# Optimization experiments

Hardware: AMD Instinct MI355X
Metric: run time of the kernel (lower is better)

Reference implementation:

```python
import jax, jax.numpy as jnp
import numpy as np

S, B, E, H, Q, T, K, N = 256, 32, 768, 1024, 64, 512, 11, 16
STD = 2.5
EPS = 1e-5


def gaussian_kernel(size, std):
    t = np.linspace(-(size - 1) / 2, (size - 1) / 2, size)
    x, y = np.meshgrid(t, t)
    kern = np.exp(-0.5 * (x ** 2 + y ** 2) / std ** 2)
    return (kern / kern.sum()).astype(np.float32)


def setup_inputs() -> dict:
    key = jax.random.key(0)
    ks = jax.random.split(key, 24)
    s = 0.05
    inp = {
        'sentence_batch': jax.random.normal(ks[0], (S, B, E), jnp.float32),
        # forward LSTM params (torch layout: W_ih (4H,E), W_hh (4H,H), gate order i,f,g,o)
        'Wih_f': jax.random.normal(ks[1], (4 * H, E), jnp.float32) * s,
        'Whh_f': jax.random.normal(ks[2], (4 * H, H), jnp.float32) * s,
        'bih_f': jnp.zeros((4 * H,), jnp.float32),
        'bhh_f': jnp.zeros((4 * H,), jnp.float32),
        # backward LSTM params
        'Wih_b': jax.random.normal(ks[3], (4 * H, E), jnp.float32) * s,
        'Whh_b': jax.random.normal(ks[4], (4 * H, H), jnp.float32) * s,
        'bih_b': jnp.zeros((4 * H,), jnp.float32),
        'bhh_b': jnp.zeros((4 * H,), jnp.float32),
        # layer norms
        'g_in': jnp.ones((E,), jnp.float32), 'be_in': jnp.zeros((E,), jnp.float32),
        'g_fw': jnp.ones((H,), jnp.float32), 'be_fw': jnp.zeros((H,), jnp.float32),
        'g_bk': jnp.ones((H,), jnp.float32), 'be_bk': jnp.zeros((H,), jnp.float32),
        'g_sq': jnp.ones((2 * Q,), jnp.float32), 'be_sq': jnp.zeros((2 * Q,), jnp.float32),
        # squeeze + topic linears (torch layout: W (out,in))
        'Wsq': jax.random.normal(ks[5], (Q, H), jnp.float32) * s,
        'bsq': jnp.zeros((Q,), jnp.float32),
        'Wtop': jax.random.normal(ks[6], (T, 2 * Q), jnp.float32) * s,
        'btop': jnp.zeros((T,), jnp.float32),
        'gauss_kern': jnp.asarray(gaussian_kernel(K, STD)),
    }
    return inp


def layer_norm(x, g, b):
    mu = jnp.mean(x, axis=-1, keepdims=True)
    var = jnp.mean((x - mu) ** 2, axis=-1, keepdims=True)
    return g * (x - mu) * jax.lax.rsqrt(var + EPS) + b


def lstm(x, Wih, Whh, bih, bhh):
    # x: (S, B, E) -> hidden states (S, B, H). torch gate order: i, f, g, o.
    h0 = jnp.zeros((x.shape[1], Whh.shape[1]), x.dtype)
    c0 = jnp.zeros_like(h0)
    xg = jnp.einsum('sbe,ge->sbg', x, Wih) + bih  # precompute input gates

    def step(carry, xt):
        h, c = carry
        gates = xt + h @ Whh.T + bhh
        i, f, g, o = jnp.split(gates, 4, axis=-1)
        c = jax.nn.sigmoid(f) * c + jax.nn.sigmoid(i) * jnp.tanh(g)
        h = jax.nn.sigmoid(o) * jnp.tanh(c)
        return (h, c), h

    _, hs = jax.lax.scan(step, (h0, c0), xg)
    return hs


def batch_pca(e, dim):
    # e: (S, B, F) -> projections (B, S, dim) onto top-dim principal axes
    c = e - jnp.mean(e, axis=0)
    cov = jnp.einsum('sbi,sbj->bij', c, c) / e.shape[0]  # (B, F, F), symmetric
    _, evecs = jnp.linalg.eigh(cov)  # ascending eigenvalues
    top = evecs[:, :, ::-1][:, :, :dim]  # (B, F, dim), descending order
    return jnp.einsum('sbf,bfn->bsn', c, top)


def gauss_smooth(x, kern):
    # x: (B, S, N) smoothed with 2D gaussian, SAME padding
    p = (kern.shape[0] - 1) // 2
    y = jax.lax.conv_general_dilated(
        x[:, None, :, :], kern[None, None, :, :], (1, 1), [(p, p), (p, p)])
    return y[:, 0]


def adj_cos(e):
    # cosine similarity between adjacent sequence positions: (B, S, N) -> (B, S-1)
    a, b = e[:, :-1], e[:, 1:]
    num = jnp.sum(a * b, axis=-1)
    den = jnp.linalg.norm(a, axis=-1) * jnp.linalg.norm(b, axis=-1)
    return num / den


def reference(sentence_batch, Wih_f, Whh_f, bih_f, bhh_f, Wih_b, Whh_b, bih_b, bhh_b,
              g_in, be_in, g_fw, be_fw, g_bk, be_bk, g_sq, be_sq,
              Wsq, bsq, Wtop, btop, gauss_kern):
    x = layer_norm(sentence_batch, g_in, be_in)
    x_f = lstm(x, Wih_f, Whh_f, bih_f, bhh_f)
    x_b = lstm(x[::-1], Wih_b, Whh_b, bih_b, bhh_b)[::-1]
    x_f = layer_norm(x_f, g_fw, be_fw)
    x_b = layer_norm(x_b, g_bk, be_bk)
    x_f = jnp.tanh(jnp.einsum('sbh,qh->sbq', x_f, Wsq) + bsq)
    x_b = jnp.tanh(jnp.einsum('sbh,qh->sbq', x_b, Wsq) + bsq)
    xc = layer_norm(jnp.concatenate((x_f, x_b), axis=-1), g_sq, be_sq)
    topic_preds = jnp.einsum('sbq,tq->sbt', xc, Wtop) + btop

    # segmentation path (no-grad in original)
    e_f = batch_pca(jax.lax.stop_gradient(x_f), N)
    e_b = batch_pca(jax.lax.stop_gradient(x_b), N)
    e_f = gauss_smooth(e_f, gauss_kern)
    e_b = gauss_smooth(e_b, gauss_kern)
    d = jnp.sqrt(adj_cos(e_f) * adj_cos(e_b))  # (B, S-1)
    pos = jnp.argmax(d, axis=1)
    return topic_preds, pos
```

## Files before the change

kernel.cpp:

```cpp
#include <hip/hip_runtime.h>
#include <cstdint>
#include <cstddef>

#define SS   256
#define BB   32
#define EE   768
#define HH   1024
#define QQ   64
#define TTOP 512
#define NPC  16
#define G4   4096
#define TCHUNK 32
#define NBLK 256
#define EPSF 1e-5f

#define OFF_XNT   ((size_t)0)
#define OFF_WHHT  ((size_t)6291456)
#define OFF_CT    ((size_t)14680064)
#define OFF_HBUF  ((size_t)14745600)
#define OFF_CNT   ((size_t)14876672)
#define OFF_XG    ((size_t)14877184)
#define OFF_HS    ((size_t)23265792)
#define OFF_XQ    ((size_t)40043008)
#define OFF_CMAT  ((size_t)0)
#define OFF_COV   ((size_t)1048576)
#define OFF_PG    ((size_t)1310720)
#define OFF_COS   ((size_t)1376256)

#define WLKS 4616
#define LSTM_DYN_LDS 153344

#define AST 65
#define EIG_DYN_LDS 133120

#define EPS32D    5.9604644775390625e-8
#define EPS232D   (EPS32D*EPS32D)
#define SAFMIN32D 1.1754943508222875e-38

__device__ __forceinline__ float sigm(float x){ return 1.0f/(1.0f + expf(-x)); }

__device__ __forceinline__ double wsumd(double v){
  #pragma unroll
  for (int o = 32; o; o >>= 1) v += __shfl_xor(v, o, 64);
  return v;
}
__device__ __forceinline__ double wmaxd(double v){
  #pragma unroll
  for (int o = 32; o; o >>= 1) v = fmax(v, __shfl_xor(v, o, 64));
  return v;
}
__device__ __forceinline__ void dlartg_(double f, double g, double& c, double& s, double& r){
  if (g == 0.0){ c = 1.0; s = 0.0; r = f; }
  else if (f == 0.0){ c = 0.0; s = (g >= 0.0) ? 1.0 : -1.0; r = fabs(g); }
  else {
    double d = sqrt(f*f + g*g);
    c = fabs(f)/d;
    r = copysign(d, f);
    s = g/r;
  }
}
__device__ void dlaev2_(double a, double b, double c,
                        double& rt1, double& rt2, double& cs1, double& sn1){
  double sm = a + c, df = a - c, adf = fabs(df), tb = b + b, ab = fabs(tb);
  double acmx, acmn;
  if (fabs(a) > fabs(c)){ acmx = a; acmn = c; } else { acmx = c; acmn = a; }
  double rt;
  if (adf > ab)      rt = adf*sqrt(1.0 + (ab/adf)*(ab/adf));
  else if (adf < ab) rt = ab*sqrt(1.0 + (adf/ab)*(adf/ab));
  else               rt = ab*sqrt(2.0);
  int sgn1;
  if (sm < 0.0){ rt1 = 0.5*(sm - rt); sgn1 = -1; rt2 = (acmx/rt1)*acmn - (b/rt1)*b; }
  else if (sm > 0.0){ rt1 = 0.5*(sm + rt); sgn1 = 1; rt2 = (acmx/rt1)*acmn - (b/rt1)*b; }
  else { rt1 = 0.5*rt; rt2 = -0.5*rt; sgn1 = 1; }
  double cs; int sgn2;
  if (df >= 0.0){ cs = df + rt; sgn2 = 1; } else { cs = df - rt; sgn2 = -1; }
  double acs = fabs(cs);
  if (acs > ab){ double ct = -tb/cs; sn1 = 1.0/sqrt(1.0+ct*ct); cs1 = ct*sn1; }
  else {
    if (ab == 0.0){ cs1 = 1.0; sn1 = 0.0; }
    else { double tn = -cs/tb; cs1 = 1.0/sqrt(1.0+tn*tn); sn1 = tn*cs1; }
  }
  if (sgn1 == sgn2){ double tn = cs1; cs1 = -sn1; sn1 = tn; }
}

__device__ void dsteqr16_(int base, double* d, double* e, double* z16, int ln,
                          double* tmpd, double* tmpz, int* rk){
  if (ln < 16){
    #pragma unroll
    for (int j = 0; j < 16; j++) z16[ln*17+j] = (ln==j) ? 1.0 : 0.0;
  }
  const int n = 16, nm1 = 15;
  int jtot = 0; const int nmaxit = 480;
  int l1 = 0;
  while (l1 < n){
    if (l1 > 0) e[base+l1-1] = 0.0;
    int m = nm1;
    for (int mm = l1; mm < nm1; mm++){
      double tst = fabs(e[base+mm]);
      if (tst == 0.0){ m = mm; break; }
      if (tst <= (sqrt(fabs(d[base+mm]))*sqrt(fabs(d[base+mm+1])))*EPS32D){
        e[base+mm] = 0.0; m = mm; break;
      }
    }
    int l = l1, lend = m;
    l1 = m + 1;
    if (lend == l) continue;
    if (fabs(d[base+lend]) < fabs(d[base+l])){ int t = l; l = lend; lend = t; }
    if (lend > l){
      for (;;){
        int mm = lend;
        for (int k2 = l; k2 < lend; k2++){
          double tst = e[base+k2]*e[base+k2];
          if (tst <= (EPS232D*fabs(d[base+k2]))*fabs(d[base+k2+1]) + SAFMIN32D){ mm = k2; break; }
        }
        if (mm < lend) e[base+mm] = 0.0;
        double p = d[base+l];
        if (mm == l){ l++; if (l <= lend) continue; break; }
        if (mm == l+1){
          double rt1, rt2, cc, ss;
          dlaev2_(d[base+l], e[base+l], d[base+l+1], rt1, rt2, cc, ss);
          if (ln < 16){
            double x = z16[ln*17+l], y = z16[ln*17+l+1];
            z16[ln*17+l]   = cc*x + ss*y;
            z16[ln*17+l+1] = cc*y - ss*x;
          }
          d[base+l] = rt1; d[base+l+1] = rt2; e[base+l] = 0.0;
          l += 2; if (l <= lend) continue; break;
        }
        if (jtot == nmaxit) break;
        jtot++;
        double g = (d[base+l+1]-p)/(2.0*e[base+l]);
        double r = sqrt(g*g+1.0);
        g = d[base+mm] - p + e[base+l]/(g + copysign(r, g));
        double s2 = 1.0, c2 = 1.0; p = 0.0;
        for (int i = mm-1; i >= l; i--){
          double f = s2*e[base+i], b = c2*e[base+i];
          dlartg_(g, f, c2, s2, r);
          if (i != mm-1) e[base+i+1] = r;
          g = d[base+i+1] - p;
          r = (d[base+i]-g)*s2 + 2.0*c2*b;
          p = s2*r;
          d[base+i+1] = g + p;
          g = c2*r - b;
          if (ln < 16){
            double x = z16[ln*17+i], y = z16[ln*17+i+1];
            z16[ln*17+i]   = c2*x - s2*y;
            z16[ln*17+i+1] = s2*x + c2*y;
          }
        }
        d[base+l] -= p; e[base+l] = g;
      }
    } else {
      for (;;){
        int mm = lend;
        for (int k2 = l; k2 > lend; k2--){
          double tst = e[base+k2-1]*e[base+k2-1];
          if (tst <= (EPS232D*fabs(d[base+k2]))*fabs(d[base+k2-1]) + SAFMIN32D){ mm = k2; break; }
        }
        if (mm > lend) e[base+mm-1] = 0.0;
        double p = d[base+l];
        if (mm == l){ l--; if (l >= lend) continue; break; }
        if (mm == l-1){
          double rt1, rt2, cc, ss;
          dlaev2_(d[base+l-1], e[base+l-1], d[base+l], rt1, rt2, cc, ss);
          if (ln < 16){
            double x = z16[ln*17+l-1], y = z16[ln*17+l];
            z16[ln*17+l-1] = cc*x + ss*y;
            z16[ln*17+l]   = cc*y - ss*x;
          }
          d[base+l-1] = rt1; d[base+l] = rt2; e[base+l-1] = 0.0;
          l -= 2; if (l >= lend) continue; break;
        }
        if (jtot == nmaxit) break;
        jtot++;
        double g = (d[base+l-1]-p)/(2.0*e[base+l-1]);
        double r = sqrt(g*g+1.0);
        g = d[base+mm] - p + e[base+l-1]/(g + copysign(r, g));
        double s2 = 1.0, c2 = 1.0; p = 0.0;
        for (int i = mm; i <= l-1; i++){
          double f = s2*e[base+i], b = c2*e[base+i];
          dlartg_(g, f, c2, s2, r);
          if (i != mm) e[base+i-1] = r;
          g = d[base+i] - p;
          r = (d[base+i+1]-g)*s2 + 2.0*c2*b;
          p = s2*r;
          d[base+i] = g + p;
          g = c2*r - b;
          if (ln < 16){
            double x = z16[ln*17+i], y = z16[ln*17+i+1];
            z16[ln*17+i]   = c2*x + s2*y;
            z16[ln*17+i+1] = c2*y - s2*x;
          }
        }
        d[base+l] -= p; e[base+l-1] = g;
      }
    }
  }
  if (ln < 16){
    double di = d[base+ln]; int r = 0;
    for (int j = 0; j < 16; j++){
      double dj = d[base+j];
      if (dj < di || (dj == di && j < ln)) r++;
    }
    rk[ln] = r;
    tmpd[r] = di;
  }
  if (ln < 16){
    for (int j = 0; j < 16; j++) tmpz[ln*16 + rk[j]] = z16[ln*17 + j];
    for (int j = 0; j < 16; j++) z16[ln*17 + j] = tmpz[ln*16 + j];
    d[base+ln] = tmpd[ln];
  }
}

__device__ void dc_merge1(int base, int n1, int n2, double rho_in, int ln,
    double* s_d, double* Zt, double* Ttp,
    double* md, double* mz, double* dl, double* wz, double* lam, double* zh,
    double* ev, double* su, int* indx, int* sec, int* defl, int* prm){
  const int n = n1 + n2;
  double zv = 0.0;
  if (ln < n){
    if (ln < n1) zv = Zt[(size_t)(base+n1-1)*AST + base + ln];
    else         zv = Zt[(size_t)(base+n1)*AST + base + ln];
    if (rho_in < 0.0 && ln >= n1) zv = -zv;
  }
  zv *= 0.70710678118654752440;
  double mdv = (ln < n) ? s_d[base+ln] : 0.0;
  if (ln < n){ mz[ln] = zv; md[ln] = mdv; }
  double rho = fabs(2.0*rho_in);
  if (ln == 0){
    int i1 = 0, i2 = n1, k = 0;
    while (i1 < n1 && i2 < n){
      if (md[i2] < md[i1]) indx[k++] = i2++; else indx[k++] = i1++;
    }
    while (i1 < n1) indx[k++] = i1++;
    while (i2 < n)  indx[k++] = i2++;
  }
  double dmax = wmaxd((ln<n) ? fabs(mdv) : 0.0);
  double zmax = wmaxd((ln<n) ? fabs(zv) : 0.0);
  double tol = 8.0*EPS32D*fmax(dmax, zmax);
  int K = 0, ndefl = 0, pj = -1;
  for (int j = 0; j < n; j++){
    int nj = indx[j];
    if (rho*fabs(mz[nj]) <= tol){
      defl[ndefl++] = nj;
    } else if (pj < 0){
      pj = nj;
    } else {
      double sG = mz[pj], cG = mz[nj];
      double tau = sqrt(cG*cG + sG*sG);
      double tdf = md[nj] - md[pj];
      double c = cG/tau, s = -sG/tau;
      if (fabs(tdf*c*s) <= tol){
        mz[nj] = tau; mz[pj] = 0.0;
        if (ln < n){
          double x = Zt[(size_t)(base+ln)*AST + base+pj];
          double y = Zt[(size_t)(base+ln)*AST + base+nj];
          Zt[(size_t)(base+ln)*AST + base+pj] = c*x + s*y;
          Zt[(size_t)(base+ln)*AST + base+nj] = c*y - s*x;
        }
        double t2 = md[pj]*c*c + md[nj]*s*s;
        double t3 = md[pj]*s*s + md[nj]*c*c;
        md[nj] = t3; md[pj] = t2;
        defl[ndefl++] = pj;
        pj = nj;
      } else {
        sec[K] = pj; dl[K] = md[pj]; wz[K] = mz[pj]; K++;
        pj = nj;
      }
    }
  }
  if (pj >= 0){ sec[K] = pj; dl[K] = md[pj]; wz[K] = mz[pj]; K++; }
  double wsum2 = wsumd((ln < K) ? wz[ln]*wz[ln] : 0.0);
  if (ln < K){
    double lo = dl[ln];
    double hi = (ln < K-1) ? dl[ln+1] : (dl[K-1] + rho*wsum2);
    for (int it = 0; it < 120; it++){
      double mid = 0.5*(lo+hi);
      if (!(mid > lo) || !(mid < hi)) break;
      double fv = 1.0;
      for (int i2 = 0; i2 < K; i2++) fv += rho*wz[i2]*wz[i2]/(dl[i2]-mid);
      if (fv < 0.0) lo = mid; else hi = mid;
    }
    double lj = 0.5*(lo+hi);
    if (!(lj > dl[ln])) lj = nextafter(dl[ln], 1.0e300);
    lam[ln] = lj;
  }
  if (ln < K){
    double di = dl[ln];
    double prod = lam[K-1] - di;
    for (int j2 = 0; j2 < ln; j2++)   prod *= (lam[j2]-di)/(dl[j2]-di);
    for (int j2 = ln; j2 < K-1; j2++) prod *= (lam[j2]-di)/(dl[j2+1]-di);
    zh[ln] = copysign(sqrt(fabs(prod)), wz[ln]);
  }
  for (int j = 0; j < K; j++){
    double ui = (ln < K) ? zh[ln]/(dl[ln]-lam[j]) : 0.0;
    double nrm = sqrt(wsumd(ui*ui));
    su[ln] = ui/nrm;
    if (ln < n){
      double acc = 0.0;
      for (int i2 = 0; i2 < K; i2++)
        acc += Zt[(size_t)(base+ln)*AST + base + sec[i2]]*su[i2];
      Ttp[(size_t)ln*AST + j] = acc;
    }
    ev[j] = lam[j];
  }
  for (int j = 0; j < ndefl; j++){
    int cj = defl[j];
    if (ln < n) Ttp[(size_t)ln*AST + K + j] = Zt[(size_t)(base+ln)*AST + base + cj];
    ev[K+j] = md[cj];
  }
  if (ln < n){
    double di = ev[ln]; int r = 0;
    for (int j2 = 0; j2 < n; j2++){
      double dj = ev[j2];
      if (dj < di || (dj == di && j2 < ln)) r++;
    }
    prm[r] = ln;
  }
  if (ln < n){
    for (int c2 = 0; c2 < n; c2++)
      Zt[(size_t)(base+ln)*AST + base + c2] = Ttp[(size_t)ln*AST + prm[c2]];
    s_d[base+ln] = ev[prm[ln]];
  }
}

__device__ void dc_merge(int base, int n1, int n2, double rho_in, int tid,
    double* s_d, double* Zt, double* Tt,
    double* md, double* mz, double* dl, double* wz, double* lam, double* zh,
    double* ev, double* su4, int* indx, int* sec, int* defl, int* prm,
    int* sKn){
  const int ln = tid & 63, w = tid >> 6;
  int n = n1 + n2;
  double zv = 0.0;
  if (ln < n){
    if (ln < n1) zv = Zt[(size_t)(base+n1-1)*AST + base + ln];
    else         zv = Zt[(size_t)(base+n1)*AST + base + ln];
    if (rho_in < 0.0 && ln >= n1) zv = -zv;
  }
  zv *= 0.70710678118654752440;
  mz[ln] = (ln < n) ? zv : 0.0;
  md[ln] = (ln < n) ? s_d[base+ln] : 0.0;
  __syncthreads();
  double rho = fabs(2.0*rho_in);
  if (tid == 0){
    int i1 = 0, i2 = n1, k = 0;
    while (i1 < n1 && i2 < n){
      if (md[i2] < md[i1]) indx[k++] = i2++; else indx[k++] = i1++;
    }
    while (i1 < n1) indx[k++] = i1++;
    while (i2 < n)  indx[k++] = i2++;
  }
  __syncthreads();
  double dmax = wmaxd((ln<n) ? fabs(md[ln]) : 0.0);
  double zmax = wmaxd((ln<n) ? fabs(mz[ln]) : 0.0);
  double tol = 8.0*EPS32D*fmax(dmax, zmax);
  if (w == 0){
    int K = 0, ndefl = 0, pj = -1;
    for (int j = 0; j < n; j++){
      int nj = indx[j];
      if (rho*fabs(mz[nj]) <= tol){
        defl[ndefl++] = nj;
      } else if (pj < 0){
        pj = nj;
      } else {
        double sG = mz[pj], cG = mz[nj];
        double tau = sqrt(cG*cG + sG*sG);
        double tdf = md[nj] - md[pj];
        double c = cG/tau, s = -sG/tau;
        if (fabs(tdf*c*s) <= tol){
          mz[nj] = tau; mz[pj] = 0.0;
          if (ln < n){
            double x = Zt[(size_t)(base+ln)*AST + base+pj];
            double y = Zt[(size_t)(base+ln)*AST + base+nj];
            Zt[(size_t)(base+ln)*AST + base+pj] = c*x + s*y;
            Zt[(size_t)(base+ln)*AST + base+nj] = c*y - s*x;
          }
          double t2 = md[pj]*c*c + md[nj]*s*s;
          double t3 = md[pj]*s*s + md[nj]*c*c;
          md[nj] = t3; md[pj] = t2;
          defl[ndefl++] = pj;
          pj = nj;
        } else {
          sec[K] = pj; dl[K] = md[pj]; wz[K] = mz[pj]; K++;
          pj = nj;
        }
      }
    }
    if (pj >= 0){ sec[K] = pj; dl[K] = md[pj]; wz[K] = mz[pj]; K++; }
    if (ln == 0){ sKn[0] = K; sKn[1] = ndefl; }
  }
  __syncthreads();
  const int K = sKn[0], ndefl = sKn[1];
  double wsum2 = wsumd((ln < K) ? wz[ln]*wz[ln] : 0.0);
  {
    bool conv = (ln >= K);
    double lo = 0.0, hi = 0.0;
    if (!conv){
      lo = dl[ln];
      hi = (ln < K-1) ? dl[ln+1] : (dl[K-1] + rho*wsum2);
    }
    const int i2lo = w*16;
    for (int it = 0; it < 120; it++){
      double mid = 0.0;
      if (!conv){
        mid = 0.5*(lo+hi);
        if (!(mid > lo) || !(mid < hi)) conv = true;
      }
      double fp = 0.0;
      if (!conv){
        int i2hi = i2lo + 16; if (i2hi > K) i2hi = K;
        for (int i2 = i2lo; i2 < i2hi; i2++)
          fp += rho*wz[i2]*wz[i2]/(dl[i2]-mid);
      }
      const int p = (it & 1)*256;
      su4[p + w*64 + ln] = fp;
      int alldone = __syncthreads_count(conv ? 1 : 0);
      if (alldone == 256) break;
      if (!conv){
        double fv = 1.0 + su4[p+ln] + su4[p+64+ln] + su4[p+128+ln] + su4[p+192+ln];
        if (fv < 0.0) lo = mid; else hi = mid;
      }
    }
    if (ln < K){
      double lj = 0.5*(lo+hi);
      if (!(lj > dl[ln])) lj = nextafter(dl[ln], 1.0e300);
      lam[ln] = lj;
    }
  }
  __syncthreads();
  if (ln < K){
    double di = dl[ln];
    double prod = lam[K-1] - di;
    for (int j2 = 0; j2 < ln; j2++)   prod *= (lam[j2]-di)/(dl[j2]-di);
    for (int j2 = ln; j2 < K-1; j2++) prod *= (lam[j2]-di)/(dl[j2+1]-di);
    zh[ln] = copysign(sqrt(fabs(prod)), wz[ln]);
  }
  __syncthreads();
  for (int j = w; j < K; j += 4){
    double ui = (ln < K) ? zh[ln]/(dl[ln]-lam[j]) : 0.0;
    double nrm = sqrt(wsumd(ui*ui));
    su4[w*64 + ln] = ui/nrm;
    if (ln < n){
      double acc = 0.0;
      for (int i2 = 0; i2 < K; i2++)
        acc += Zt[(size_t)(base+ln)*AST + base + sec[i2]]*su4[w*64 + i2];
      Tt[(size_t)ln*AST + j] = acc;
    }
    if (ln == 0) ev[j] = lam[j];
  }
  __syncthreads();
  for (int j = 0; j < ndefl; j++){
    int cj = defl[j];
    if (ln < n) Tt[(size_t)ln*AST + K + j] = Zt[(size_t)(base+ln)*AST + base + cj];
    if (ln == 0) ev[K+j] = md[cj];
  }
  __syncthreads();
  if (w == 0 && ln < n){
    double di = ev[ln]; int r = 0;
    for (int j2 = 0; j2 < n; j2++){
      double dj = ev[j2];
      if (dj < di || (dj == di && j2 < ln)) r++;
    }
    prm[r] = ln;
  }
  __syncthreads();
  if (ln < n){
    for (int c2 = 0; c2 < n; c2++)
      Zt[(size_t)(base+ln)*AST + base + c2] = Tt[(size_t)ln*AST + prm[c2]];
  }
  if (ln == 0){ for (int c2 = 0; c2 < n; c2++) s_d[base+c2] = ev[prm[c2]]; }
  __syncthreads();
}

__global__ __launch_bounds__(256) void k_eig(const float* __restrict__ covg,
                                             float* __restrict__ Pg){
  int u = blockIdx.x, tid = threadIdx.x;
  const int ln = tid & 63, w = tid >> 6;
  extern __shared__ double dsm[];
  double* A  = dsm;
  double* Qh = dsm + 4160;
  double* Zt = dsm + 8320;
  double* Tt = dsm + 12480;
  __shared__ double s_d[64], s_e[64], s_tau[64], s_v[64], s_w[64];
  __shared__ double md[64], mz[64], dl[64], wz[64], lam[64], zh[64], ev[64];
  __shared__ double su4[2*4*64];
  __shared__ double z16a[4*272];
  __shared__ int indx[64], sec[64], defl[64], prm[64], sKn[2];

  for (int n = tid; n < 4096; n += 256)
    A[(n >> 6)*AST + (n & 63)] = (double)covg[(size_t)u*4096 + n];
  __syncthreads();

  for (int i = 0; i < 63; i++){
    double alpha = A[(size_t)(i+1)*AST + i];
    double xv = (ln >= i+2) ? A[(size_t)ln*AST + i] : 0.0;
    double xnorm2 = wsumd(xv*xv);
    if (xnorm2 == 0.0){
      if (tid == 0){ s_e[i] = alpha; s_tau[i] = 0.0; }
    } else {
      double beta = -copysign(sqrt(alpha*alpha + xnorm2), alpha);
      double taui = (beta - alpha)/beta;
      double sc = 1.0/(alpha - beta);
      s_v[ln] = (ln == i+1) ? 1.0 : ((ln >= i+2) ? A[(size_t)ln*AST+i]*sc : 0.0);
      __syncthreads();
      if (ln >= i+2) A[(size_t)ln*AST+i] = s_v[ln];
      double wr = 0.0;
      if (ln >= i+1){
        for (int c2 = i+1; c2 < 64; c2++){
          double av = (ln >= c2) ? A[(size_t)ln*AST+c2] : A[(size_t)c2*AST+ln];
          wr += av*s_v[c2];
        }
        wr *= taui;
      }
      double dotwv = wsumd((ln >= i+1) ? wr*s_v[ln] : 0.0);
      double alp2 = -0.5*taui*dotwv;
      wr += alp2*s_v[ln];
      s_w[ln] = (ln >= i+1) ? wr : 0.0;
      __syncthreads();
      if (ln >= i+1){
        for (int c2 = i+1; c2 <= ln; c2++)
          if ((c2 & 3) == w)
            A[(size_t)ln*AST+c2] -= s_v[ln]*s_w[c2] + s_w[ln]*s_v[c2];
      }
      if (tid == 0){ s_e[i] = beta; s_tau[i] = taui; }
    }
    __syncthreads();
  }
  if (w == 0) s_d[ln] = A[(size_t)ln*AST+ln];
  __syncthreads();

  for (int n = tid; n < 4160; n += 256) Qh[n] = 0.0;
  __syncthreads();
  if (w == 0) Qh[(size_t)ln*AST+ln] = 1.0;
  __syncthreads();
  for (int i = 62; i >= 0; i--){
    double taui = s_tau[i];
    if (taui != 0.0){
      s_v[ln] = (ln == i+1) ? 1.0 : ((ln >= i+2) ? A[(size_t)ln*AST+i] : 0.0);
      __syncthreads();
      double dj = 0.0;
      for (int r2 = i+1; r2 < 64; r2++) dj += s_v[r2]*Qh[(size_t)r2*AST+ln];
      dj *= taui;
      for (int r2 = i+1; r2 < 64; r2++)
        if ((r2 & 3) == w)
          Qh[(size_t)r2*AST+ln] -= s_v[r2]*dj;
    }
    __syncthreads();
  }

  double rho_a = s_e[15], rho_b = s_e[47], rho_top = s_e[31];
  if (tid == 0){
    s_d[15] -= fabs(rho_a);   s_d[16] -= fabs(rho_a);
    s_d[31] -= fabs(rho_top); s_d[32] -= fabs(rho_top);
    s_d[47] -= fabs(rho_b);   s_d[48] -= fabs(rho_b);
  }
  for (int n = tid; n < 4160; n += 256) Zt[n] = 0.0;
  __syncthreads();
  dsteqr16_(w*16, s_d, s_e, &z16a[w*272], ln,
            &su4[w*64], Tt + (size_t)w*1040, &indx[w*16]);
  if (ln < 16){
    for (int j = 0; j < 16; j++)
      Zt[(size_t)(w*16+ln)*AST + w*16 + j] = z16a[w*272 + ln*17+j];
  }
  __syncthreads();

  if (w == 0)
    dc_merge1(0, 16, 16, rho_a, ln, s_d, Zt, Tt,
              md, mz, dl, wz, lam, zh, ev, su4,
              indx, sec, defl, prm);
  else if (w == 1)
    dc_merge1(32, 16, 16, rho_b, ln, s_d, Zt, Tt + (size_t)32*AST,
              md+32, mz+32, dl+32, wz+32, lam+32, zh+32, ev+32, su4+64,
              indx+32, sec+32, defl+32, prm+32);
  __syncthreads();

  dc_merge(0, 32, 32, rho_top, tid, s_d, Zt, Tt, md, mz, dl, wz, lam, zh, ev, su4, indx, sec, defl, prm, sKn);

  for (int nn = w; nn < 16; nn += 4){
    double acc = 0.0;
    for (int k = 0; k < 64; k++)
      acc += Qh[(size_t)ln*AST+k]*Zt[(size_t)k*AST + (63-nn)];
    Pg[(size_t)u*1024 + ln*16 + nn] = (float)acc;
  }
}

__global__ void k_ln_in(const float* __restrict__ x, const float* __restrict__ g,
                        const float* __restrict__ be, float* __restrict__ xnT){
  int bid = blockIdx.x; int s = bid >> 5, b = bid & 31;
  int tid = threadIdx.x;
  const float* row = x + ((size_t)(s*BB + b))*EE;
  __shared__ float r1[256], r2[256];
  float su = 0.f, sq = 0.f;
  for (int e = tid; e < EE; e += 256){ float v = row[e]; su += v; sq += v*v; }
  r1[tid] = su; r2[tid] = sq; __syncthreads();
  for (int st = 128; st > 0; st >>= 1){
    if (tid < st){ r1[tid] += r1[tid+st]; r2[tid] += r2[tid+st]; }
    __syncthreads();
  }
  float mu  = r1[0] * (1.0f/EE);
  float var = r2[0] * (1.0f/EE) - mu*mu;
  float rstd = rsqrtf(var + EPSF);
  for (int e = tid; e < EE; e += 256){
    float v = (row[e]-mu)*rstd*g[e] + be[e];
    xnT[((size_t)s*EE + e)*BB + b] = v;
  }
}

__global__ void k_whht(const float* __restrict__ Whh_f, const float* __restrict__ Whh_b,
                       float* __restrict__ WhhT){
  int d  = blockIdx.z;
  const float* Whh = d ? Whh_b : Whh_f;
  int rt = blockIdx.x*32, kt = blockIdx.y*32;
  int tx = threadIdx.x & 31, ty = threadIdx.x >> 5;
  __shared__ float tile[32][33];
  for (int i = ty; i < 32; i += 8)
    tile[i][tx] = Whh[(size_t)(rt+i)*HH + kt+tx];
  __syncthreads();
  for (int i = ty; i < 32; i += 8)
    WhhT[((size_t)d*HH + kt+i)*G4 + rt+tx] = tile[tx][i];
}

__global__ void k_zero(float* __restrict__ p, int n){
  int i = blockIdx.x*blockDim.x + threadIdx.x;
  if (i < n) p[i] = 0.f;
}

__global__ __launch_bounds__(256) void k_xg(const float* __restrict__ xnT,
        const float* __restrict__ Wih_f, const float* __restrict__ Wih_b,
        float* __restrict__ xg, int* __restrict__ cnt, int c){
  if (blockIdx.x == 0 && blockIdx.y == 0){
    if (threadIdx.x < 17)
      __hip_atomic_store(&cnt[threadIdx.x*16], 0, __ATOMIC_RELAXED, __HIP_MEMORY_SCOPE_AGENT);
    else if (threadIdx.x == 17)
      __hip_atomic_store(&cnt[384], 0, __ATOMIC_RELAXED, __HIP_MEMORY_SCOPE_AGENT);
  }
  int nb = blockIdx.x, rb = blockIdx.y;
  int d = rb >> 5, rloc0 = (rb & 31)*128;
  const float* Wih = d ? Wih_b : Wih_f;
  int tid = threadIdx.x;
  int tx = tid & 15, ty = tid >> 4;
  __shared__ float Al[16*132];
  __shared__ float Bl[16*132];
  float acc[8][8];
  #pragma unroll
  for (int i = 0; i < 8; i++)
    #pragma unroll
    for (int j = 0; j < 8; j++) acc[i][j] = 0.f;
  for (int kc = 0; kc < EE; kc += 16){
    #pragma unroll
    for (int j = 0; j < 8; j++){
      int idx = tid + j*256;
      int n = idx & 127, k = idx >> 7;
      int tglob = c*TCHUNK + nb*4 + (n >> 5);
      int tsrc = d ? (SS-1-tglob) : tglob;
      Al[k*132 + n] = xnT[((size_t)tsrc*EE + kc + k)*BB + (n & 31)];
    }
    #pragma unroll
    for (int j = 0; j < 8; j++){
      int idx = tid + j*256;
      int k = idx & 15, r = idx >> 4;
      Bl[k*132 + r] = Wih[(size_t)(rloc0 + r)*EE + kc + k];
    }
    __syncthreads();
    #pragma unroll
    for (int k = 0; k < 16; k++){
      float4 a0 = *(const float4*)(&Al[k*132 + tx*4]);
      float4 a1 = *(const float4*)(&Al[k*132 + 64 + tx*4]);
      float4 b0 = *(const float4*)(&Bl[k*132 + ty*4]);
      float4 b1 = *(const float4*)(&Bl[k*132 + 64 + ty*4]);
      float av[8] = {a0.x,a0.y,a0.z,a0.w,a1.x,a1.y,a1.z,a1.w};
      float bv[8] = {b0.x,b0.y,b0.z,b0.w,b1.x,b1.y,b1.z,b1.w};
      #pragma unroll
      for (int i = 0; i < 8; i++)
        #pragma unroll
        for (int j2 = 0; j2 < 8; j2++) acc[i][j2] += av[i]*bv[j2];
    }
    __syncthreads();
  }
  #pragma unroll
  for (int j = 0; j < 8; j++){
    int r = rloc0 + ((j < 4) ? (ty*4 + j) : (64 + ty*4 + j - 4));
    #pragma unroll
    for (int ig = 0; ig < 2; ig++){
      int n0 = ig*64 + tx*4;
      int tl = nb*4 + (n0 >> 5), b = n0 & 31;
      float4 o = make_float4(acc[ig*4+0][j], acc[ig*4+1][j], acc[ig*4+2][j], acc[ig*4+3][j]);
      *(float4*)(&xg[(((size_t)tl*8192) + d*G4 + r)*BB + b]) = o;
    }
  }
}

__global__ __launch_bounds__(512) void k_lstm(
    const float* __restrict__ WhhT,
    const float* __restrict__ bih_f, const float* __restrict__ bhh_f,
    const float* __restrict__ bih_b, const float* __restrict__ bhh_b,
    const float* __restrict__ xg, float* __restrict__ hbuf,
    float* __restrict__ cT, float* __restrict__ hs,
    int* __restrict__ cnt, int c)
{
  extern __shared__ float lsm[];
  float* Wl  = lsm;
  float* gl  = lsm + 36928;
  float* cls = lsm + 38080;

  const int blk = blockIdx.x;
  const int d   = blk >> 7;
  const int j0  = (blk & 127) * 8;
  const int tid = threadIdx.x;
  const int ln  = tid & 63;
  const int w   = tid >> 6;
  const int ksub = ln >> 3;
  const int bg   = ln & 7;
  const int b0   = bg * 4;
  const int cbase = w * 4;

  const float* bih = d ? bih_b : bih_f;
  const float* bhh = d ? bhh_b : bhh_f;
  const float* WT_d = WhhT + (size_t)d * HH * G4;

  {
    const int cs = tid & 31;
    const int ks = tid >> 5;
    const int g  = cs >> 3, jj = cs & 7;
    const size_t rglob = (size_t)g*HH + j0 + jj;
    for (int kk = 0; kk < 64; kk++){
      int k = kk*16 + ks;
      Wl[(k >> 7)*WLKS + (k & 127)*36 + cs] = WT_d[(size_t)k*G4 + rglob];
    }
  }

  const int pjj = (tid >> 5) & 7, pb = tid & 31;
  float pbias[4];
  if (tid < 256){
    cls[pjj*32 + pb] = cT[((size_t)d*HH + j0 + pjj)*BB + pb];
    #pragma unroll
    for (int g2 = 0; g2 < 4; g2++)
      pbias[g2] = bih[g2*HH + j0 + pjj] + bhh[g2*HH + j0 + pjj];
  }
  __syncthreads();

  for (int tl = 0; tl < TCHUNK; tl++){
    const int s = c*TCHUNK + tl;
    const float* hprev = hbuf + ((size_t)((s & 1)*2 + d))*HH*BB;
    float*       hnext = hbuf + ((size_t)(((s+1) & 1)*2 + d))*HH*BB;

    float xgv[4] = {0.f,0.f,0.f,0.f};
    if (tid < 256){
      const size_t xbase = ((size_t)tl*8192 + (size_t)d*G4)*BB;
      #pragma unroll
      for (int g2 = 0; g2 < 4; g2++)
        xgv[g2] = xg[xbase + (size_t)(g2*HH + j0 + pjj)*BB + pb];
    }

    float acc[4][4];
    #pragma unroll
    for (int i = 0; i < 4; i++)
      #pragma unroll
      for (int j = 0; j < 4; j++) acc[i][j] = 0.f;

    {
      const float* hp = hprev + (size_t)(ksub*128)*BB + b0;
      const float* wrow = &Wl[ksub*WLKS + cbase];
      for (int ib = 0; ib < 128; ib += 16){
        float4 hv[16];
        #pragma unroll
        for (int u = 0; u < 16; u++)
          hv[u] = *(const float4*)(hp + (size_t)(ib+u)*BB);
        #pragma unroll
        for (int u = 0; u < 16; u++){
          float4 wv = *(const float4*)(wrow + (ib+u)*36);
          acc[0][0] += wv.x*hv[u].x; acc[0][1] += wv.x*hv[u].y; acc[0][2] += wv.x*hv[u].z; acc[0][3] += wv.x*hv[u].w;
          acc[1][0] += wv.y*hv[u].x; acc[1][1] += wv.y*hv[u].y; acc[1][2] += wv.y*hv[u].z; acc[1][3] += wv.y*hv[u].w;
          acc[2][0] += wv.z*hv[u].x; acc[2][1] += wv.z*hv[u].y; acc[2][2] += wv.z*hv[u].z; acc[2][3] += wv.z*hv[u].w;
          acc[3][0] += wv.w*hv[u].x; acc[3][1] += wv.w*hv[u].y; acc[3][2] += wv.w*hv[u].z; acc[3][3] += wv.w*hv[u].w;
        }
      }
    }
    #pragma unroll
    for (int i = 0; i < 4; i++)
      #pragma unroll
      for (int j = 0; j < 4; j++){
        float v = acc[i][j];
        v += __shfl_xor(v, 8, 64);
        v += __shfl_xor(v, 16, 64);
        v += __shfl_xor(v, 32, 64);
        acc[i][j] = v;
      }
    if (ksub == 0){
      #pragma unroll
      for (int i = 0; i < 4; i++){
        float4 o = make_float4(acc[i][0], acc[i][1], acc[i][2], acc[i][3]);
        *(float4*)(&gl[(cbase + i)*36 + b0]) = o;
      }
    }
    __syncthreads();
    if (tid < 256){
      float gv[4];
      #pragma unroll
      for (int g2 = 0; g2 < 4; g2++)
        gv[g2] = gl[(g2*8 + pjj)*36 + pb] + pbias[g2] + xgv[g2];
      float iv = sigm(gv[0]), fv = sigm(gv[1]), ggv = tanhf(gv[2]), ov = sigm(gv[3]);
      float cv = fv*cls[pjj*32 + pb] + iv*ggv;
      cls[pjj*32 + pb] = cv;
      float h = ov*tanhf(cv);
      hnext[(size_t)(j0 + pjj)*BB + pb] = h;
      int tsv = d ? (SS-1-s) : s;
      hs[(((size_t)d*SS + tsv)*HH + j0 + pjj)*BB + pb] = h;
    }
    if (tl < TCHUNK-1){
      __syncthreads();
      if (tid == 0){
        __builtin_amdgcn_fence(__ATOMIC_RELEASE, "agent");
        __hip_atomic_fetch_add(&cnt[((blk & 7) + d*8)*16], 1, __ATOMIC_RELAXED, __HIP_MEMORY_SCOPE_AGENT);
        const int target = 16*(tl+1);
        const int flagidx = d ? 384 : 256;
        if ((blk & 127) == 0){
          const int lbase = d*8;
          int done = 0;
          while (done < 8){
            done = 0;
            #pragma unroll
            for (int i = 0; i < 8; i++)
              done += (__hip_atomic_load(&cnt[(lbase+i)*16], __ATOMIC_RELAXED, __HIP_MEMORY_SCOPE_AGENT) >= target);
            if (done < 8) __builtin_amdgcn_s_sleep(2);
          }
          __hip_atomic_store(&cnt[flagidx], tl+1, __ATOMIC_RELAXED, __HIP_MEMORY_SCOPE_AGENT);
        } else {
          while (__hip_atomic_load(&cnt[flagidx], __ATOMIC_RELAXED, __HIP_MEMORY_SCOPE_AGENT) < tl+1)
            __builtin_amdgcn_s_sleep(2);
        }
        __builtin_amdgcn_fence(__ATOMIC_ACQUIRE, "agent");
      }
      __syncthreads();
    }
  }
  __syncthreads();
  if (tid < 256)
    cT[((size_t)d*HH + j0 + pjj)*BB + pb] = cls[pjj*32 + pb];
}

__global__ __launch_bounds__(256) void k_lnproj(const float* __restrict__ hs,
        const float* __restrict__ g_fw, const float* __restrict__ be_fw,
        const float* __restrict__ g_bk, const float* __restrict__ be_bk,
        const float* __restrict__ Wsq, const float* __restrict__ bsq,
        float* __restrict__ xq){
  int t = blockIdx.x, d = blockIdx.y;
  int tid = threadIdx.x;
  const float* gv  = d ? g_bk  : g_fw;
  const float* bev = d ? be_bk : be_fw;
  const float* hrow = hs + ((size_t)d*SS + t)*HH*BB;
  __shared__ float red[256], red2[256];
  __shared__ float smu[32], srs[32];
  __shared__ float ln[32*132];
  __shared__ float wl[64*132];
  {
    int b = tid & 31, jg = tid >> 5;
    float s = 0.f, s2 = 0.f;
    for (int j = jg*128; j < jg*128+128; j++){
      float v = hrow[(size_t)j*BB + b];
      s += v; s2 += v*v;
    }
    red[b*8 + jg] = s; red2[b*8 + jg] = s2; __syncthreads();
    if (tid < 32){
      float a = 0.f, a2 = 0.f;
      for (int k = 0; k < 8; k++){ a += red[tid*8+k]; a2 += red2[tid*8+k]; }
      float mu = a*(1.f/HH), var = a2*(1.f/HH) - mu*mu;
      smu[tid] = mu; srs[tid] = rsqrtf(var + EPSF);
    }
    __syncthreads();
  }
  float acc[4][2] = {{0.f,0.f},{0.f,0.f},{0.f,0.f},{0.f,0.f}};
  int qg = tid & 31, bg = tid >> 5;
  int q0 = qg*2, b0g = bg*4;
  for (int jc = 0; jc < 8; jc++){
    for (int n = tid; n < 4096; n += 256){
      int b = n & 31, jj = n >> 5; int j = jc*128 + jj;
      float v = hrow[(size_t)j*BB + b];
      ln[b*132+jj] = (v - smu[b])*srs[b]*gv[j] + bev[j];
    }
    for (int n = tid; n < 8192; n += 256){
      int q = n >> 7, jj = n & 127;
      wl[q*132+jj] = Wsq[(size_t)q*HH + jc*128 + jj];
    }
    __syncthreads();
    for (int jj = 0; jj < 128; jj += 4){
      float4 w0 = *(const float4*)(&wl[q0*132+jj]);
      float4 w1 = *(const float4*)(&wl[(q0+1)*132+jj]);
      #pragma unroll
      for (int i = 0; i < 4; i++){
        float4 xv = *(const float4*)(&ln[(b0g+i)*132+jj]);
        acc[i][0] += xv.x*w0.x + xv.y*w0.y + xv.z*w0.z + xv.w*w0.w;
        acc[i][1] += xv.x*w1.x + xv.y*w1.y + xv.z*w1.z + xv.w*w1.w;
      }
    }
    __syncthreads();
  }
  #pragma unroll
  for (int i = 0; i < 4; i++)
    #pragma unroll
    for (int u = 0; u < 2; u++){
      float o = tanhf(acc[i][u] + bsq[q0+u]);
      xq[(((size_t)d*SS + t)*BB + (b0g+i))*QQ + q0 + u] = o;
    }
}

__global__ __launch_bounds__(256) void k_topic(const float* __restrict__ xq,
        const float* __restrict__ g_sq, const float* __restrict__ be_sq,
        const float* __restrict__ Wtop, const float* __restrict__ btop,
        float* __restrict__ out){
  int t = blockIdx.x; int tid = threadIdx.x;
  __shared__ float xc[32*132];
  __shared__ float wl[16*520];
  __shared__ float red[256], red2[256];
  __shared__ float smu[32], srs[32];
  for (int n = tid; n < 4096; n += 256){
    int b = n >> 7, q = n & 127;
    float v = (q < 64) ? xq[(((size_t)0*SS + t)*BB + b)*QQ + q]
                       : xq[(((size_t)1*SS + t)*BB + b)*QQ + (q-64)];
    xc[b*132+q] = v;
  }
  __syncthreads();
  {
    int b = tid >> 3, sl = tid & 7;
    float s = 0.f, s2 = 0.f;
    for (int k = 0; k < 16; k++){ float v = xc[b*132 + sl*16 + k]; s += v; s2 += v*v; }
    red[tid] = s; red2[tid] = s2; __syncthreads();
    if (tid < 32){
      float a = 0.f, a2 = 0.f;
      for (int k = 0; k < 8; k++){ a += red[tid*8+k]; a2 += red2[tid*8+k]; }
      float mu = a*(1.f/128.f), var = a2*(1.f/128.f) - mu*mu;
      smu[tid] = mu; srs[tid] = rsqrtf(var + EPSF);
    }
    __syncthreads();
    for (int n = tid; n < 4096; n += 256){
      int b2 = n >> 7, q = n & 127;
      xc[b2*132+q] = (xc[b2*132+q]-smu[b2])*srs[b2]*g_sq[q] + be_sq[q];
    }
    __syncthreads();
  }
  int og = tid & 63, bg = tid >> 6;
  int o0 = og*8, b0 = bg*8;
  float acc[8][8];
  #pragma unroll
  for (int i = 0; i < 8; i++)
    #pragma unroll
    for (int j = 0; j < 8; j++) acc[i][j] = 0.f;
  for (int kc = 0; kc < 128; kc += 16){
    for (int n = tid; n < 8192; n += 256){
      int o = n >> 4, kk = n & 15;
      wl[kk*520 + o] = Wtop[(size_t)o*128 + kc + kk];
    }
    __syncthreads();
    #pragma unroll
    for (int kk = 0; kk < 16; kk++){
      float4 w0 = *(const float4*)(&wl[kk*520+o0]);
      float4 w1 = *(const float4*)(&wl[kk*520+o0+4]);
      float wv[8] = {w0.x,w0.y,w0.z,w0.w,w1.x,w1.y,w1.z,w1.w};
      int k = kc + kk;
      #pragma unroll
      for (int bi = 0; bi < 8; bi++){
        float xv = xc[(b0+bi)*132 + k];
        #pragma unroll
        for (int oi = 0; oi < 8; oi++) acc[bi][oi] += xv*wv[oi];
      }
    }
    __syncthreads();
  }
  #pragma unroll
  for (int bi = 0; bi < 8; bi++){
    int b = b0 + bi;
    #pragma unroll
    for (int oi = 0; oi < 8; oi++)
      out[((size_t)t*BB + b)*TTOP + o0 + oi] = acc[bi][oi] + btop[o0+oi];
  }
}

__global__ __launch_bounds__(256) void k_pca1(const float* __restrict__ xq,
        float* __restrict__ cmat, float* __restrict__ covg){
  int u = blockIdx.x; int d = u >> 5, b = u & 31;
  int tid = threadIdx.x;
  __shared__ float red[256];
  __shared__ float smq[64];
  {
    int q = tid & 63, tg = tid >> 6;
    float s = 0.f;
    for (int t2 = tg*64; t2 < tg*64+64; t2++)
      s += xq[(((size_t)d*SS + t2)*BB + b)*QQ + q];
    red[tid] = s; __syncthreads();
    if (tid < 64) smq[tid] = (red[tid]+red[tid+64]+red[tid+128]+red[tid+192])*(1.f/SS);
    __syncthreads();
  }
  float* cm = cmat + (size_t)u*SS*QQ;
  for (int n = tid; n < SS*QQ; n += 256){
    int t2 = n >> 6, q = n & 63;
    cm[n] = xq[(((size_t)d*SS + t2)*BB + b)*QQ + q] - smq[q];
  }
  __syncthreads();
  {
    int pg = (tid & 15)*4, qg = (tid >> 4)*4;
    float a[4][4] = {{0}};
    for (int t2 = 0; t2 < SS; t2++){
      const float* cr = cm + (size_t)t2*QQ;
      float4 cp = *(const float4*)(cr+pg);
      float4 cq = *(const float4*)(cr+qg);
      float pv[4] = {cp.x,cp.y,cp.z,cp.w}, qv[4] = {cq.x,cq.y,cq.z,cq.w};
      #pragma unroll
      for (int i = 0; i < 4; i++)
        #pragma unroll
        for (int j2 = 0; j2 < 4; j2++) a[i][j2] += pv[i]*qv[j2];
    }
    #pragma unroll
    for (int i = 0; i < 4; i++)
      #pragma unroll
      for (int j2 = 0; j2 < 4; j2++)
        covg[(size_t)u*4096 + (pg+i)*64 + qg+j2] = a[i][j2]*(1.f/SS);
  }
}

__global__ __launch_bounds__(256) void k_pca2(const float* __restrict__ cmat,
        const float* __restrict__ Pg, const float* __restrict__ kern,
        float* __restrict__ cosb){
  int u = blockIdx.x; int tid = threadIdx.x;
  __shared__ float sP[1024];
  __shared__ float sE[4096];
  __shared__ float sY[4096];
  __shared__ float kb[121];
  __shared__ float nn2[256];
  if (tid < 121) kb[tid] = kern[tid];
  for (int n = tid; n < 1024; n += 256) sP[n] = Pg[(size_t)u*1024 + n];
  __syncthreads();
  const float* cm = cmat + (size_t)u*SS*QQ;
  for (int m = tid; m < SS*NPC; m += 256){
    int t2 = m >> 4, n = m & 15;
    const float* cr = cm + (size_t)t2*QQ;
    float acc = 0.f;
    for (int i = 0; i < 64; i++) acc += cr[i]*sP[i*16+n];
    sE[m] = acc;
  }
  __syncthreads();
  for (int m = tid; m < SS*NPC; m += 256){
    int t2 = m >> 4, n = m & 15;
    float acc = 0.f;
    for (int a2 = 0; a2 < 11; a2++){
      int ta = t2 + a2 - 5;
      if (ta < 0 || ta >= SS) continue;
      #pragma unroll
      for (int b2 = 0; b2 < 11; b2++){
        int nb = n + b2 - 5;
        if (nb < 0 || nb >= NPC) continue;
        acc += kb[a2*11+b2]*sE[ta*16+nb];
      }
    }
    sY[m] = acc;
  }
  __syncthreads();
  {
    float acc = 0.f;
    #pragma unroll
    for (int n = 0; n < 16; n++){ float v = sY[tid*16+n]; acc += v*v; }
    nn2[tid] = acc;
  }
  __syncthreads();
  if (tid < 255){
    float num = 0.f;
    #pragma unroll
    for (int n = 0; n < 16; n++) num += sY[tid*16+n]*sY[(tid+1)*16+n];
    cosb[(size_t)u*256 + tid] = num/(sqrtf(nn2[tid])*sqrtf(nn2[tid+1]));
  }
}

__global__ void k_pos(const float* __restrict__ cosb, float* __restrict__ out){
  __shared__ float mx[256];
  __shared__ int   mi[256];
  int tid = threadIdx.x;
  for (int b = 0; b < 32; b++){
    float v = -1e30f;
    if (tid < 255){
      float cf = cosb[(size_t)(b)*256 + tid];
      float cb = cosb[(size_t)(32+b)*256 + tid];
      v = sqrtf(cf*cb);
      if (isnan(v)) v = INFINITY;
    }
    mx[tid] = v; __syncthreads();
    for (int st = 128; st > 0; st >>= 1){
      if (tid < st) mx[tid] = fmaxf(mx[tid], mx[tid+st]);
      __syncthreads();
    }
    float m = mx[0]; __syncthreads();
    mi[tid] = (tid < 255 && v == m) ? tid : (1<<30);
    __syncthreads();
    for (int st = 128; st > 0; st >>= 1){
      if (tid < st) mi[tid] = min(mi[tid], mi[tid+st]);
      __syncthreads();
    }
    if (tid == 0) out[(size_t)SS*BB*TTOP + b] = (float)mi[0];
    __syncthreads();
  }
}

extern "C" void kernel_launch(void* const* d_in, const int* in_sizes, int n_in,
                              void* d_out, int out_size, void* d_ws, size_t ws_size,
                              hipStream_t stream){
  (void)in_sizes; (void)n_in; (void)out_size; (void)ws_size;
  const float* x      = (const float*)d_in[0];
  const float* Wih_f  = (const float*)d_in[1];
  const float* Whh_f  = (const float*)d_in[2];
  const float* bih_f  = (const float*)d_in[3];
  const float* bhh_f  = (const float*)d_in[4];
  const float* Wih_b  = (const float*)d_in[5];
  const float* Whh_b  = (const float*)d_in[6];
  const float* bih_b  = (const float*)d_in[7];
  const float* bhh_b  = (const float*)d_in[8];
  const float* g_in   = (const float*)d_in[9];
  const float* be_in  = (const float*)d_in[10];
  const float* g_fw   = (const float*)d_in[11];
  const float* be_fw  = (const float*)d_in[12];
  const float* g_bk   = (const float*)d_in[13];
  const float* be_bk  = (const float*)d_in[14];
  const float* g_sq   = (const float*)d_in[15];
  const float* be_sq  = (const float*)d_in[16];
  const float* Wsq    = (const float*)d_in[17];
  const float* bsq    = (const float*)d_in[18];
  const float* Wtop   = (const float*)d_in[19];
  const float* btop   = (const float*)d_in[20];
  const float* gkern  = (const float*)d_in[21];

  float* ws    = (float*)d_ws;
  float* xnT   = ws + OFF_XNT;
  float* WhhT  = ws + OFF_WHHT;
  float* cT    = ws + OFF_CT;
  float* hbuf  = ws + OFF_HBUF;
  int*   cnt   = (int*)(ws + OFF_CNT);
  float* xg    = ws + OFF_XG;
  float* hs    = ws + OFF_HS;
  float* xq    = ws + OFF_XQ;
  float* cmat  = ws + OFF_CMAT;
  float* covg  = ws + OFF_COV;
  float* Pg    = ws + OFF_PG;
  float* cosb  = ws + OFF_COS;
  float* out   = (float*)d_out;

  hipFuncSetAttribute((const void*)k_eig,
                      hipFuncAttributeMaxDynamicSharedMemorySize, EIG_DYN_LDS);
  hipFuncSetAttribute((const void*)k_lstm,
                      hipFuncAttributeMaxDynamicSharedMemorySize, LSTM_DYN_LDS);

  k_zero<<<dim3(768), dim3(256), 0, stream>>>(cT, 196608);
  k_ln_in<<<dim3(SS*BB), dim3(256), 0, stream>>>(x, g_in, be_in, xnT);
  k_whht<<<dim3(128, 32, 2), dim3(256), 0, stream>>>(Whh_f, Whh_b, WhhT);
  for (int c = 0; c < SS/TCHUNK; c++){
    k_xg<<<dim3(8, 64), dim3(256), 0, stream>>>(xnT, Wih_f, Wih_b, xg, cnt, c);
    k_lstm<<<dim3(NBLK), dim3(512), LSTM_DYN_LDS, stream>>>(WhhT, bih_f, bhh_f, bih_b, bhh_b,
                                                            xg, hbuf, cT, hs, cnt, c);
  }
  k_lnproj<<<dim3(SS,2), dim3(256), 0, stream>>>(hs, g_fw, be_fw, g_bk, be_bk, Wsq, bsq, xq);
  k_topic<<<dim3(SS), dim3(256), 0, stream>>>(xq, g_sq, be_sq, Wtop, btop, out);
  k_pca1<<<dim3(64), dim3(256), 0, stream>>>(xq, cmat, covg);
  k_eig<<<dim3(64), dim3(256), EIG_DYN_LDS, stream>>>(covg, Pg);
  k_pca2<<<dim3(64), dim3(256), 0, stream>>>(cmat, Pg, gkern, cosb);
  k_pos<<<dim3(1), dim3(256), 0, stream>>>(cosb, out);
}
```

Baseline: 7.268 ms.

## Fuse next-chunk input projection into LSTM steps and flatten grid barrier

```diff
diff --git a/kernel.cpp b/kernel.cpp
--- a/kernel.cpp
+++ b/kernel.cpp
@@ -11,6 +11,7 @@
 #define NPC  16
 #define G4   4096
 #define TCHUNK 32
+#define NCH  (SS/TCHUNK)
 #define NBLK 256
 #define EPSF 1e-5f
 
@@ -628,12 +629,8 @@
 __global__ __launch_bounds__(256) void k_xg(const float* __restrict__ xnT,
         const float* __restrict__ Wih_f, const float* __restrict__ Wih_b,
         float* __restrict__ xg, int* __restrict__ cnt, int c){
-  if (blockIdx.x == 0 && blockIdx.y == 0){
-    if (threadIdx.x < 17)
-      __hip_atomic_store(&cnt[threadIdx.x*16], 0, __ATOMIC_RELAXED, __HIP_MEMORY_SCOPE_AGENT);
-    else if (threadIdx.x == 17)
-      __hip_atomic_store(&cnt[384], 0, __ATOMIC_RELAXED, __HIP_MEMORY_SCOPE_AGENT);
-  }
+  if (blockIdx.x == 0 && blockIdx.y == 0 && threadIdx.x < 16)
+    __hip_atomic_store(&cnt[threadIdx.x*16], 0, __ATOMIC_RELAXED, __HIP_MEMORY_SCOPE_AGENT);
   int nb = blockIdx.x, rb = blockIdx.y;
   int d = rb >> 5, rloc0 = (rb & 31)*128;
   const float* Wih = d ? Wih_b : Wih_f;
@@ -692,9 +689,11 @@
 
 __global__ __launch_bounds__(512) void k_lstm(
     const float* __restrict__ WhhT,
+    const float* __restrict__ Wih_f, const float* __restrict__ Wih_b,
+    const float* __restrict__ xnT,
     const float* __restrict__ bih_f, const float* __restrict__ bhh_f,
     const float* __restrict__ bih_b, const float* __restrict__ bhh_b,
-    const float* __restrict__ xg, float* __restrict__ hbuf,
+    float* __restrict__ xg, float* __restrict__ hbuf,
     float* __restrict__ cT, float* __restrict__ hs,
     int* __restrict__ cnt, int c)
 {
@@ -708,15 +707,15 @@
   const int j0  = (blk & 127) * 8;
   const int tid = threadIdx.x;
   const int ln  = tid & 63;
-  const int w   = tid >> 6;
   const int ksub = ln >> 3;
   const int bg   = ln & 7;
   const int b0   = bg * 4;
-  const int cbase = w * 4;
+  const int cbase = (tid >> 6) * 4;
 
   const float* bih = d ? bih_b : bih_f;
   const float* bhh = d ? bhh_b : bhh_f;
   const float* WT_d = WhhT + (size_t)d * HH * G4;
+  const float* Wih_d = d ? Wih_b : Wih_f;
 
   {
     const int cs = tid & 31;
@@ -737,6 +736,10 @@
     for (int g2 = 0; g2 < 4; g2++)
       pbias[g2] = bih[g2*HH + j0 + pjj] + bhh[g2*HH + j0 + pjj];
   }
+  const int prl = tid >> 4;
+  const int prglob = (prl >> 3)*HH + j0 + (prl & 7);
+  const int pb2 = (tid & 15)*2;
+  const float* wihrow = Wih_d + (size_t)prglob*EE;
   __syncthreads();
 
   for (int tl = 0; tl < TCHUNK; tl++){
@@ -807,27 +810,39 @@
       int tsv = d ? (SS-1-s) : s;
       hs[(((size_t)d*SS + tsv)*HH + j0 + pjj)*BB + pb] = h;
     }
+    if (c < NCH-1){
+      const int tglob = (c+1)*TCHUNK + tl;
+      const int tsrc2 = d ? (SS-1-tglob) : tglob;
+      const float* xnp = xnT + (size_t)tsrc2*EE*BB + pb2;
+      float a0 = 0.f, a1 = 0.f;
+      for (int k = 0; k < EE; k += 4){
+        float4 wv = *(const float4*)(wihrow + k);
+        float2 x0 = *(const float2*)(xnp + (size_t)k*BB);
+        float2 x1 = *(const float2*)(xnp + (size_t)(k+1)*BB);
+        float2 x2 = *(const float2*)(xnp + (size_t)(k+2)*BB);
+        float2 x3 = *(const float2*)(xnp + (size_t)(k+3)*BB);
+        a0 += wv.x*x0.x; a1 += wv.x*x0.y;
+        a0 += wv.y*x1.x; a1 += wv.y*x1.y;
+        a0 += wv.z*x2.x; a1 += wv.z*x2.y;
+        a0 += wv.w*x3.x; a1 += wv.w*x3.y;
+      }
+      float* xo = xg + ((size_t)tl*8192 + (size_t)d*G4 + prglob)*BB + pb2;
+      xo[0] = a0; xo[1] = a1;
+    }
     if (tl < TCHUNK-1){
       __syncthreads();
       if (tid == 0){
         __builtin_amdgcn_fence(__ATOMIC_RELEASE, "agent");
         __hip_atomic_fetch_add(&cnt[((blk & 7) + d*8)*16], 1, __ATOMIC_RELAXED, __HIP_MEMORY_SCOPE_AGENT);
-        const int target = 16*(tl+1);
-        const int flagidx = d ? 384 : 256;
-        if ((blk & 127) == 0){
-          const int lbase = d*8;
-          int done = 0;
-          while (done < 8){
-            done = 0;
-            #pragma unroll
-            for (int i = 0; i < 8; i++)
-              done += (__hip_atomic_load(&cnt[(lbase+i)*16], __ATOMIC_RELAXED, __HIP_MEMORY_SCOPE_AGENT) >= target);
-            if (done < 8) __builtin_amdgcn_s_sleep(2);
-          }
-          __hip_atomic_store(&cnt[flagidx], tl+1, __ATOMIC_RELAXED, __HIP_MEMORY_SCOPE_AGENT);
-        } else {
-          while (__hip_atomic_load(&cnt[flagidx], __ATOMIC_RELAXED, __HIP_MEMORY_SCOPE_AGENT) < tl+1)
-            __builtin_amdgcn_s_sleep(2);
+        const int target = 16*(c*(TCHUNK-1) + tl + 1);
+        const int lbase = d*8;
+        int done = 0;
+        while (done < 8){
+          done = 0;
+          #pragma unroll
+          for (int i = 0; i < 8; i++)
+            done += (__hip_atomic_load(&cnt[(lbase+i)*16], __ATOMIC_RELAXED, __HIP_MEMORY_SCOPE_AGENT) >= target);
+          if (done < 8) __builtin_amdgcn_s_sleep(2);
         }
         __builtin_amdgcn_fence(__ATOMIC_ACQUIRE, "agent");
       }
@@ -1148,9 +1163,10 @@
   k_zero<<<dim3(768), dim3(256), 0, stream>>>(cT, 196608);
   k_ln_in<<<dim3(SS*BB), dim3(256), 0, stream>>>(x, g_in, be_in, xnT);
   k_whht<<<dim3(128, 32, 2), dim3(256), 0, stream>>>(Whh_f, Whh_b, WhhT);
-  for (int c = 0; c < SS/TCHUNK; c++){
-    k_xg<<<dim3(8, 64), dim3(256), 0, stream>>>(xnT, Wih_f, Wih_b, xg, cnt, c);
-    k_lstm<<<dim3(NBLK), dim3(512), LSTM_DYN_LDS, stream>>>(WhhT, bih_f, bhh_f, bih_b, bhh_b,
+  k_xg<<<dim3(8, 64), dim3(256), 0, stream>>>(xnT, Wih_f, Wih_b, xg, cnt, 0);
+  for (int c = 0; c < NCH; c++){
+    k_lstm<<<dim3(NBLK), dim3(512), LSTM_DYN_LDS, stream>>>(WhhT, Wih_f, Wih_b, xnT,
+                                                            bih_f, bhh_f, bih_b, bhh_b,
                                                             xg, hbuf, cT, hs, cnt, c);
   }
   k_lnproj<<<dim3(SS,2), dim3(256), 0, stream>>>(hs, g_fw, be_fw, g_bk, be_bk, Wsq, bsq, xq);
```

After: 17.71 ms. 2.44x slower.
